# Kernel tuning notes

Hardware: AMD Instinct MI355X
Metric: run time of the kernel (lower is better)

The kernel has to match this reference:

```python
import jax, jax.numpy as jnp
import numpy as np

B, T, F = 1024, 256, 64
H1, H2, H3 = 64, 32, 16


def _lstm_params(key, in_dim, units, scale=0.1):
    k1, k2, k3 = jax.random.split(key, 3)
    W = jax.random.normal(k1, (in_dim, 4 * units), jnp.float32) * scale
    U = jax.random.normal(k2, (units, 4 * units), jnp.float32) * scale
    b = jax.random.normal(k3, (4 * units,), jnp.float32) * scale
    return W, U, b


def lstm_seq(x, W, U, b, reverse):
    """Keras-style LSTM (gate order i,f,g,o). Returns (all_h [B,T,H] time-aligned, last_h [B,H])."""
    Bx = x.shape[0]
    H = U.shape[0]
    xz = jnp.einsum('bti,ij->btj', x, W) + b  # [B,T,4H]
    if reverse:
        xz = xz[:, ::-1]
    xz = jnp.swapaxes(xz, 0, 1)  # [T,B,4H]

    def step(carry, zx):
        h, c = carry
        z = zx + h @ U
        i, f, g, o = jnp.split(z, 4, axis=-1)
        i = jax.nn.sigmoid(i)
        f = jax.nn.sigmoid(f)
        g = jnp.tanh(g)
        o = jax.nn.sigmoid(o)
        c = f * c + i * g
        h = o * jnp.tanh(c)
        return (h, c), h

    h0 = jnp.zeros((Bx, H), x.dtype)
    (hT, _), hs = jax.lax.scan(step, (h0, h0), xz)
    hs = jnp.swapaxes(hs, 0, 1)  # [B,T,H]
    if reverse:
        hs = hs[:, ::-1]  # Keras Bidirectional re-reverses backward outputs
    return hs, hT


def setup_inputs() -> dict:
    key = jax.random.key(0)
    ks = jax.random.split(key, 10)
    x = jax.random.normal(ks[0], (B, T, F), jnp.float32)
    W1f, U1f, b1f = _lstm_params(ks[1], F, H1)
    W1b, U1b, b1b = _lstm_params(ks[2], F, H1)
    W2f, U2f, b2f = _lstm_params(ks[3], 2 * H1, H2)
    W2b, U2b, b2b = _lstm_params(ks[4], 2 * H1, H2)
    W3f, U3f, b3f = _lstm_params(ks[5], 2 * H2, H3)
    W3b, U3b, b3b = _lstm_params(ks[6], 2 * H2, H3)
    Wd1 = jax.random.normal(ks[7], (2 * H3, 16), jnp.float32) * 0.1
    bd1 = jnp.zeros((16,), jnp.float32)
    Wd2 = jax.random.normal(ks[8], (16, 2), jnp.float32) * 0.1
    bd2 = jnp.zeros((2,), jnp.float32)
    return dict(inputs=x,
                W1f=W1f, U1f=U1f, b1f=b1f, W1b=W1b, U1b=U1b, b1b=b1b,
                W2f=W2f, U2f=U2f, b2f=b2f, W2b=W2b, U2b=U2b, b2b=b2b,
                W3f=W3f, U3f=U3f, b3f=b3f, W3b=W3b, U3b=U3b, b3b=b3b,
                Wd1=Wd1, bd1=bd1, Wd2=Wd2, bd2=bd2)


def reference(inputs,
              W1f, U1f, b1f, W1b, U1b, b1b,
              W2f, U2f, b2f, W2b, U2b, b2b,
              W3f, U3f, b3f, W3b, U3b, b3b,
              Wd1, bd1, Wd2, bd2):
    # inference path: all dropout / GaussianDropout layers are identity
    hf, _ = lstm_seq(inputs, W1f, U1f, b1f, reverse=False)
    hb, _ = lstm_seq(inputs, W1b, U1b, b1b, reverse=True)
    x = jnp.concatenate([hf, hb], axis=-1)  # [B,T,128]

    hf, _ = lstm_seq(x, W2f, U2f, b2f, reverse=False)
    hb, _ = lstm_seq(x, W2b, U2b, b2b, reverse=True)
    x = jnp.concatenate([hf, hb], axis=-1)  # [B,T,64]

    _, hf_last = lstm_seq(x, W3f, U3f, b3f, reverse=False)
    _, hb_last = lstm_seq(x, W3b, U3b, b3b, reverse=True)
    x = jnp.concatenate([hf_last, hb_last], axis=-1)  # [B,32] (Flatten is identity)

    x = jnp.clip(x @ Wd1 + bd1, 0.0, 6.0)  # relu6
    logits = x @ Wd2 + bd2
    return jax.nn.softmax(logits, axis=-1)
```

## Files before the change

### kernel.cpp

```cpp
#include <hip/hip_runtime.h>
#include <hip/hip_bf16.h>

#define T_SEQ 256
#define BATCH 1024

typedef __attribute__((ext_vector_type(8))) short  short8;
typedef __attribute__((ext_vector_type(4))) float  floatx4;
typedef unsigned short ushort_t;
typedef unsigned int   uint_t;

template <int P> struct IC { static constexpr int v = P; };

constexpr float NL2E = -1.4426950408889634f;
constexpr float L2E2 =  2.8853900817779268f;

__device__ __forceinline__ float exp2_fast(float x) {
    float r; asm("v_exp_f32 %0, %1" : "=v"(r) : "v"(x)); return r;
}
__device__ __forceinline__ float rcp_fast(float x) {
    float r; asm("v_rcp_f32 %0, %1" : "=v"(r) : "v"(x)); return r;
}
__device__ __forceinline__ ushort_t f2bf(float f) {
    union { float f; uint_t u; } v; v.f = f;
    uint_t r = v.u + 0x7FFFu + ((v.u >> 16) & 1u);
    return (ushort_t)(r >> 16);
}
__device__ __forceinline__ uint_t pk_bf16(float a, float b) {
    union { __hip_bfloat162 h; uint_t u; } v;
    v.h = __float22bfloat162_rn(make_float2(a, b));
    return v.u;
}
__device__ __forceinline__ void sync_lds() {
    asm volatile("s_waitcnt lgkmcnt(0)\n\ts_barrier" ::: "memory");
}


__device__ __forceinline__ void sig4(const float z[4], float o[4]) {
    const float A0 = 1.0f + exp2_fast(z[0]);
    const float A1 = 1.0f + exp2_fast(z[1]);
    const float A2 = 1.0f + exp2_fast(z[2]);
    const float A3 = 1.0f + exp2_fast(z[3]);
    const float P01 = A0 * A1, P23 = A2 * A3;
    const float R   = rcp_fast(P01 * P23);
    const float R01 = R * P23;
    const float R23 = R * P01;
    o[0] = R01 * A1; o[1] = R01 * A0;
    o[2] = R23 * A3; o[3] = R23 * A2;
}
__device__ __forceinline__ void tanh4(const float z[4], float o[4]) {
    float s[4]; sig4(z, s);
#pragma unroll
    for (int r = 0; r < 4; r++) o[r] = fmaf(-2.0f, s[r], 1.0f);
}

template <int D, int H, bool IS_FIRST, bool SEQ_OUT, int MODE>
__global__ __launch_bounds__(64 * (H / 16), 1) void lstm_fused(
    const void* __restrict__ xin,
    const float* __restrict__ Wf, const float* __restrict__ Uf, const float* __restrict__ bgf,
    const float* __restrict__ Wb, const float* __restrict__ Ub, const float* __restrict__ bgb,
    void* __restrict__ outp)
{
    constexpr bool SW = (MODE >= 1);
    constexpr int UG  = H / 16;
    constexpr int KSx = D / 32;
    constexpr int KSh = (H + 31) / 32;
    constexpr int HP  = (H < 32 ? 32 : H) + 8;
    constexpr int G4  = 4 * H;
    constexpr int NTH = 64 * UG;
    static_assert(D % 32 == 0 && T_SEQ % 4 == 0, "shape");

    const int tid  = threadIdx.x;
    const int ug   = tid >> 6;
    const int lane = tid & 63;
    const int lm   = lane & 15;
    const int lq   = lane >> 4;
    const int dir  = blockIdx.y;
    const int b0   = blockIdx.x * 16;

    const float* W  = dir ? Wb  : Wf;
    const float* U  = dir ? Ub  : Uf;
    const float* bg = dir ? bgb : bgf;

    __shared__ __align__(16) ushort_t hbuf[2 * 16 * HP];

    short8  aw[4][KSx];
    short8  hw[4][KSh];
    floatx4 bias4[4];
#pragma unroll
    for (int g = 0; g < 4; g++) {
        const float sc = (g == 2) ? L2E2 : NL2E;
        const int ub = g * H + ug * 16;
        floatx4 b4;
#pragma unroll
        for (int r = 0; r < 4; r++)
            b4[r] = sc * bg[ub + (SW ? lq * 4 + r : lm)];
        bias4[g] = b4;
        const int nc = ub + lm;
#pragma unroll
        for (int ks = 0; ks < KSx; ks++) {
            short8 f;
#pragma unroll
            for (int e = 0; e < 8; e++)
                f[e] = (short)f2bf(sc * W[(ks * 32 + lq * 8 + e) * G4 + nc]);
            aw[g][ks] = f;
        }
#pragma unroll
        for (int ks = 0; ks < KSh; ks++) {
            short8 f;
#pragma unroll
            for (int e = 0; e < 8; e++) {
                const int k = ks * 32 + lq * 8 + e;
                f[e] = (k < H) ? (short)f2bf(sc * U[k * G4 + nc]) : (short)0;
            }
            hw[g][ks] = f;
        }
    }

    for (int idx = tid; idx < 2 * 16 * HP; idx += NTH)
        hbuf[idx] = 0;

    float cst[4];
    float hl[4];
#pragma unroll
    for (int r = 0; r < 4; r++) { cst[r] = 0.f; hl[r] = 0.f; }

    const int t0 = dir ? T_SEQ - 1 : 0;
    const float*    pxf = (const float*)xin + ((size_t)(b0 + lm) * T_SEQ + t0) * D + lq * 8;
    const ushort_t* pxb = (const ushort_t*)xin + ((size_t)t0 * BATCH + b0 + lm) * D + lq * 8;
    const long xstepf = dir ? -(long)D : (long)D;
    const long xstepb = (dir ? -(long)BATCH : (long)BATCH) * D;
    ushort_t* pout;
    if constexpr (SW)
        pout = (ushort_t*)outp + ((size_t)t0 * BATCH + b0 + lm) * (2 * H) + dir * H +
               ug * 16 + lq * 4;
    else
        pout = (ushort_t*)outp + ((size_t)t0 * BATCH + b0 + lq * 4) * (2 * H) + dir * H +
               ug * 16 + lm;
    const long ostep = (dir ? -(long)BATCH : (long)BATCH) * (2 * H);

    float4 rawf[4][2 * KSx];
    short8 rawb[4][KSx];

    auto load_slot = [&](auto sl_) {
        constexpr int SL = decltype(sl_)::v;
        if (IS_FIRST) {
#pragma unroll
            for (int ks = 0; ks < KSx; ks++) {
                rawf[SL][2 * ks + 0] = *(const float4*)(pxf + ks * 32 + 0);
                rawf[SL][2 * ks + 1] = *(const float4*)(pxf + ks * 32 + 4);
            }
            pxf += xstepf;
        } else {
#pragma unroll
            for (int ks = 0; ks < KSx; ks++)
                rawb[SL][ks] = *(const short8*)(pxb + ks * 32);
            pxb += xstepb;
        }
    };

    load_slot(IC<0>{}); load_slot(IC<1>{}); load_slot(IC<2>{}); load_slot(IC<3>{});
    __syncthreads();

    auto step = [&](auto p_, auto sl_, int s) {
        constexpr int P  = decltype(p_)::v;
        constexpr int SL = decltype(sl_)::v;

        short8 fh[KSh];
#pragma unroll
        for (int ks = 0; ks < KSh; ks++)
            fh[ks] = *(const short8*)&hbuf[(P * 16 + lm) * HP + ks * 32 + lq * 8];

        short8 av[KSx];
        if (IS_FIRST) {
#pragma unroll
            for (int ks = 0; ks < KSx; ks++) {
                union { short8 s; uint_t u[4]; } f;
                const float* ra = (const float*)&rawf[SL][2 * ks];
#pragma unroll
                for (int e = 0; e < 4; e++) f.u[e] = pk_bf16(ra[2 * e], ra[2 * e + 1]);
                av[ks] = f.s;
            }
        } else {
#pragma unroll
            for (int ks = 0; ks < KSx; ks++) av[ks] = rawb[SL][ks];
        }

        floatx4 acc[4];
#pragma unroll
        for (int g = 0; g < 4; g++)
            acc[g] = SW
                ? __builtin_amdgcn_mfma_f32_16x16x32_bf16(aw[g][0], av[0], bias4[g], 0, 0, 0)
                : __builtin_amdgcn_mfma_f32_16x16x32_bf16(av[0], aw[g][0], bias4[g], 0, 0, 0);
#pragma unroll
        for (int ks = 1; ks < KSx; ks++)
#pragma unroll
            for (int g = 0; g < 4; g++)
                acc[g] = SW
                    ? __builtin_amdgcn_mfma_f32_16x16x32_bf16(aw[g][ks], av[ks], acc[g], 0, 0, 0)
                    : __builtin_amdgcn_mfma_f32_16x16x32_bf16(av[ks], aw[g][ks], acc[g], 0, 0, 0);

        if (s + 4 < T_SEQ) load_slot(sl_);

#pragma unroll
        for (int ks = 0; ks < KSh; ks++)
#pragma unroll
            for (int g = 0; g < 4; g++)
                acc[g] = SW
                    ? __builtin_amdgcn_mfma_f32_16x16x32_bf16(hw[g][ks], fh[ks], acc[g], 0, 0, 0)
                    : __builtin_amdgcn_mfma_f32_16x16x32_bf16(fh[ks], hw[g][ks], acc[g], 0, 0, 0);

        float zi[4], zf[4], zg[4], zo[4];
#pragma unroll
        for (int r = 0; r < 4; r++) {
            zi[r] = acc[0][r]; zf[r] = acc[1][r];
            zg[r] = acc[2][r]; zo[r] = acc[3][r];
        }
        float gi[4], gf[4], gg[4], go[4];
        sig4(zi, gi); sig4(zf, gf); tanh4(zg, gg); sig4(zo, go);
        float cz[4];
#pragma unroll
        for (int r = 0; r < 4; r++) {
            cst[r] = fmaf(gf[r], cst[r], L2E2 * (gi[r] * gg[r]));
            cz[r] = cst[r];
        }
        float tc[4];
        tanh4(cz, tc);
        float hv[4];
#pragma unroll
        for (int r = 0; r < 4; r++) hv[r] = go[r] * tc[r];

        if constexpr (SW) {
            const uint_t d0 = pk_bf16(hv[0], hv[1]);
            const uint_t d1 = pk_bf16(hv[2], hv[3]);
            uint2 wv; wv.x = d0; wv.y = d1;
            *(uint2*)&hbuf[((P ^ 1) * 16 + lm) * HP + ug * 16 + lq * 4] = wv;
            if (SEQ_OUT) {
                uint2 ov; ov.x = d0; ov.y = d1;
                *(uint2*)&pout[0] = ov;
            } else {
#pragma unroll
                for (int r = 0; r < 4; r++) hl[r] = hv[r];
            }
        } else {
#pragma unroll
            for (int r = 0; r < 4; r++) {
                const ushort_t hw_ = f2bf(hv[r]);
                hbuf[((P ^ 1) * 16 + lq * 4 + r) * HP + ug * 16 + lm] = hw_;
                if (SEQ_OUT) pout[r * 2 * H] = hw_;
                else         hl[r] = hv[r];
            }
        }
        pout += ostep;
        if (UG > 1) sync_lds();
    };

    for (int s = 0; s < T_SEQ; s += 4) {
        step(IC<0>{}, IC<0>{}, s);
        step(IC<1>{}, IC<1>{}, s + 1);
        step(IC<0>{}, IC<2>{}, s + 2);
        step(IC<1>{}, IC<3>{}, s + 3);
    }

    if (!SEQ_OUT) {
        float* op = (float*)outp;
        if constexpr (SW) {
            float4 v4 = make_float4(hl[0], hl[1], hl[2], hl[3]);
            *(float4*)&op[(size_t)(b0 + lm) * (2 * H) + dir * H + ug * 16 + lq * 4] = v4;
        } else {
#pragma unroll
            for (int r = 0; r < 4; r++)
                op[(size_t)(b0 + lq * 4 + r) * (2 * H) + dir * H + ug * 16 + lm] = hl[r];
        }
    }
}

__global__ __launch_bounds__(256) void dense_head(
    const float* __restrict__ h3, const float* __restrict__ Wd1, const float* __restrict__ bd1,
    const float* __restrict__ Wd2, const float* __restrict__ bd2, float* __restrict__ out)
{
    const int b = blockIdx.x * blockDim.x + threadIdx.x;
    if (b >= BATCH) return;
    float x[32];
#pragma unroll
    for (int k = 0; k < 32; k++) x[k] = h3[b * 32 + k];
    float y[16];
#pragma unroll
    for (int jj = 0; jj < 16; jj++) {
        float a = bd1[jj];
#pragma unroll
        for (int k = 0; k < 32; k++) a = fmaf(x[k], Wd1[k * 16 + jj], a);
        y[jj] = fminf(fmaxf(a, 0.0f), 6.0f);
    }
    float l0 = bd2[0], l1 = bd2[1];
#pragma unroll
    for (int k = 0; k < 16; k++) {
        l0 = fmaf(y[k], Wd2[k * 2 + 0], l0);
        l1 = fmaf(y[k], Wd2[k * 2 + 1], l1);
    }
    const float m = fmaxf(l0, l1);
    const float e0 = __expf(l0 - m), e1 = __expf(l1 - m);
    const float inv = 1.0f / (e0 + e1);
    out[b * 2 + 0] = e0 * inv;
    out[b * 2 + 1] = e1 * inv;
}

extern "C" void kernel_launch(void* const* d_in, const int* in_sizes, int n_in,
                              void* d_out, int out_size, void* d_ws, size_t ws_size,
                              hipStream_t stream)
{
    const float* x   = (const float*)d_in[0];
    const float* W1f = (const float*)d_in[1];
    const float* U1f = (const float*)d_in[2];
    const float* b1f = (const float*)d_in[3];
    const float* W1b = (const float*)d_in[4];
    const float* U1b = (const float*)d_in[5];
    const float* b1b = (const float*)d_in[6];
    const float* W2f = (const float*)d_in[7];
    const float* U2f = (const float*)d_in[8];
    const float* b2f = (const float*)d_in[9];
    const float* W2b = (const float*)d_in[10];
    const float* U2b = (const float*)d_in[11];
    const float* b2b = (const float*)d_in[12];
    const float* W3f = (const float*)d_in[13];
    const float* U3f = (const float*)d_in[14];
    const float* b3f = (const float*)d_in[15];
    const float* W3b = (const float*)d_in[16];
    const float* U3b = (const float*)d_in[17];
    const float* b3b = (const float*)d_in[18];
    const float* Wd1 = (const float*)d_in[19];
    const float* bd1 = (const float*)d_in[20];
    const float* Wd2 = (const float*)d_in[21];
    const float* bd2 = (const float*)d_in[22];

    char* ws = (char*)d_ws;
    void*  l1out = (void*)ws;
    void*  l2out = (void*)(ws + (size_t)64 * 1024 * 1024);
    float* h3    = (float*)(ws + (size_t)96 * 1024 * 1024);
    float* out   = (float*)d_out;

    dim3 grid(BATCH / 16, 2);

    lstm_fused<64, 64, true, true, 0>
        <<<grid, 256, 0, stream>>>(x, W1f, U1f, b1f, W1b, U1b, b1b, l1out);
    lstm_fused<128, 32, false, true, 1>
        <<<grid, 128, 0, stream>>>(l1out, W2f, U2f, b2f, W2b, U2b, b2b, l2out);
    lstm_fused<64, 16, false, false, 1>
        <<<grid, 64, 0, stream>>>(l2out, W3f, U3f, b3f, W3b, U3b, b3b, h3);
    dense_head<<<dim3(BATCH / 256), 256, 0, stream>>>(h3, Wd1, bd1, Wd2, bd2, out);
}
```

Baseline: 497.4 us.

## Add single-wave layer-3 LSTM kernel exchanging h via bpermute; per-element activations in layer 1

Adds a dedicated layer-3 kernel for the single-wave case. It passes the hidden state between lanes through ds_bpermute instead of an LDS buffer with barriers, and folds the bias into the MFMA accumulator init. It also adds an ACT template switch: layer 1 computes each sigmoid/tanh with its own reciprocal instead of the shared-reciprocal sig4 trick. This spends more transcendental instructions in exchange for shorter dependency chains. The new layer-3 path depends on the l2out layout being time-major bf16 and assumes the bpermute lane mapping matches the MFMA B-fragment layout.

```diff
diff --git a/kernel.cpp b/kernel.cpp
--- a/kernel.cpp
+++ b/kernel.cpp
@@ -53,7 +53,7 @@
     for (int r = 0; r < 4; r++) o[r] = fmaf(-2.0f, s[r], 1.0f);
 }
 
-template <int D, int H, bool IS_FIRST, bool SEQ_OUT, int MODE>
+template <int D, int H, bool IS_FIRST, bool SEQ_OUT, int MODE, int ACT>
 __global__ __launch_bounds__(64 * (H / 16), 1) void lstm_fused(
     const void* __restrict__ xin,
     const float* __restrict__ Wf, const float* __restrict__ Uf, const float* __restrict__ bgf,
@@ -209,25 +209,38 @@
                     ? __builtin_amdgcn_mfma_f32_16x16x32_bf16(hw[g][ks], fh[ks], acc[g], 0, 0, 0)
                     : __builtin_amdgcn_mfma_f32_16x16x32_bf16(fh[ks], hw[g][ks], acc[g], 0, 0, 0);
 
-        float zi[4], zf[4], zg[4], zo[4];
-#pragma unroll
-        for (int r = 0; r < 4; r++) {
-            zi[r] = acc[0][r]; zf[r] = acc[1][r];
-            zg[r] = acc[2][r]; zo[r] = acc[3][r];
-        }
-        float gi[4], gf[4], gg[4], go[4];
-        sig4(zi, gi); sig4(zf, gf); tanh4(zg, gg); sig4(zo, go);
-        float cz[4];
-#pragma unroll
-        for (int r = 0; r < 4; r++) {
-            cst[r] = fmaf(gf[r], cst[r], L2E2 * (gi[r] * gg[r]));
-            cz[r] = cst[r];
-        }
-        float tc[4];
-        tanh4(cz, tc);
         float hv[4];
-#pragma unroll
-        for (int r = 0; r < 4; r++) hv[r] = go[r] * tc[r];
+        if constexpr (ACT == 0) {
+#pragma unroll
+            for (int r = 0; r < 4; r++) {
+                const float gi = rcp_fast(1.0f + exp2_fast(acc[0][r]));
+                const float gf = rcp_fast(1.0f + exp2_fast(acc[1][r]));
+                const float gg = 1.0f - 2.0f * rcp_fast(1.0f + exp2_fast(acc[2][r]));
+                const float go = rcp_fast(1.0f + exp2_fast(acc[3][r]));
+                cst[r] = fmaf(gf, cst[r], L2E2 * (gi * gg));
+                const float tc = 1.0f - 2.0f * rcp_fast(1.0f + exp2_fast(cst[r]));
+                hv[r] = go * tc;
+            }
+        } else {
+            float zi[4], zf[4], zg[4], zo[4];
+#pragma unroll
+            for (int r = 0; r < 4; r++) {
+                zi[r] = acc[0][r]; zf[r] = acc[1][r];
+                zg[r] = acc[2][r]; zo[r] = acc[3][r];
+            }
+            float gi[4], gf[4], gg[4], go[4];
+            sig4(zi, gi); sig4(zf, gf); tanh4(zg, gg); sig4(zo, go);
+            float cz[4];
+#pragma unroll
+            for (int r = 0; r < 4; r++) {
+                cst[r] = fmaf(gf[r], cst[r], L2E2 * (gi[r] * gg[r]));
+                cz[r] = cst[r];
+            }
+            float tc[4];
+            tanh4(cz, tc);
+#pragma unroll
+            for (int r = 0; r < 4; r++) hv[r] = go[r] * tc[r];
+        }
 
         if constexpr (SW) {
             const uint_t d0 = pk_bf16(hv[0], hv[1]);
@@ -272,6 +285,136 @@
                 op[(size_t)(b0 + lq * 4 + r) * (2 * H) + dir * H + ug * 16 + lm] = hl[r];
         }
     }
+}
+
+template <int D, int H>
+__global__ __launch_bounds__(64, 1) void lstm_l3(
+    const ushort_t* __restrict__ xin,
+    const float* __restrict__ Wf, const float* __restrict__ Uf, const float* __restrict__ bgf,
+    const float* __restrict__ Wb, const float* __restrict__ Ub, const float* __restrict__ bgb,
+    float* __restrict__ outp)
+{
+    constexpr int KSx = D / 32;
+    constexpr int G4  = 4 * H;
+    static_assert(D % 32 == 0 && H == 16 && T_SEQ % 4 == 0, "l3 shape");
+
+    const int lane = threadIdx.x & 63;
+    const int lm   = lane & 15;
+    const int lq   = lane >> 4;
+    const int dir  = blockIdx.y;
+    const int b0   = blockIdx.x * 16;
+
+    const float* W  = dir ? Wb  : Wf;
+    const float* U  = dir ? Ub  : Uf;
+    const float* bg = dir ? bgb : bgf;
+
+    short8  aw[4][KSx];
+    short8  hw[4];
+    floatx4 bias4[4];
+#pragma unroll
+    for (int g = 0; g < 4; g++) {
+        const float sc = (g == 2) ? L2E2 : NL2E;
+        floatx4 b4;
+#pragma unroll
+        for (int r = 0; r < 4; r++) b4[r] = sc * bg[g * H + lq * 4 + r];
+        bias4[g] = b4;
+        const int nc = g * H + lm;
+#pragma unroll
+        for (int ks = 0; ks < KSx; ks++) {
+            short8 f;
+#pragma unroll
+            for (int e = 0; e < 8; e++)
+                f[e] = (short)f2bf(sc * W[(ks * 32 + lq * 8 + e) * G4 + nc]);
+            aw[g][ks] = f;
+        }
+        short8 f;
+#pragma unroll
+        for (int e = 0; e < 8; e++) {
+            const int k = lq * 8 + e;
+            f[e] = (k < H) ? (short)f2bf(sc * U[k * G4 + nc]) : (short)0;
+        }
+        hw[g] = f;
+    }
+
+    const int ia = (lm + 32 * (lq & 1)) * 4;
+    const int ib = ia + 64;
+
+    uint_t d0 = 0, d1 = 0;
+    float cst[4] = {0.f, 0.f, 0.f, 0.f};
+    float hl[4]  = {0.f, 0.f, 0.f, 0.f};
+
+    const int t0 = dir ? T_SEQ - 1 : 0;
+    const ushort_t* pxb = xin + ((size_t)t0 * BATCH + b0 + lm) * D + lq * 8;
+    const long xstepb = (dir ? -(long)BATCH : (long)BATCH) * D;
+
+    short8 rawb[4][KSx];
+    auto load_slot = [&](auto sl_) {
+        constexpr int SL = decltype(sl_)::v;
+#pragma unroll
+        for (int ks = 0; ks < KSx; ks++)
+            rawb[SL][ks] = *(const short8*)(pxb + ks * 32);
+        pxb += xstepb;
+    };
+    load_slot(IC<0>{}); load_slot(IC<1>{}); load_slot(IC<2>{}); load_slot(IC<3>{});
+
+    auto step = [&](auto sl_, int s) {
+        constexpr int SL = decltype(sl_)::v;
+
+        union { uint_t u[4]; short8 s8; } fr;
+        fr.u[0] = (uint_t)__builtin_amdgcn_ds_bpermute(ia, (int)d0);
+        fr.u[1] = (uint_t)__builtin_amdgcn_ds_bpermute(ia, (int)d1);
+        fr.u[2] = (uint_t)__builtin_amdgcn_ds_bpermute(ib, (int)d0);
+        fr.u[3] = (uint_t)__builtin_amdgcn_ds_bpermute(ib, (int)d1);
+
+        floatx4 acc[4];
+#pragma unroll
+        for (int g = 0; g < 4; g++)
+            acc[g] = __builtin_amdgcn_mfma_f32_16x16x32_bf16(aw[g][0], rawb[SL][0], bias4[g], 0, 0, 0);
+#pragma unroll
+        for (int ks = 1; ks < KSx; ks++)
+#pragma unroll
+            for (int g = 0; g < 4; g++)
+                acc[g] = __builtin_amdgcn_mfma_f32_16x16x32_bf16(aw[g][ks], rawb[SL][ks], acc[g], 0, 0, 0);
+
+        if (s + 4 < T_SEQ) load_slot(sl_);
+
+#pragma unroll
+        for (int g = 0; g < 4; g++)
+            acc[g] = __builtin_amdgcn_mfma_f32_16x16x32_bf16(hw[g], fr.s8, acc[g], 0, 0, 0);
+
+        float zi[4], zf[4], zg[4], zo[4];
+#pragma unroll
+        for (int r = 0; r < 4; r++) {
+            zi[r] = acc[0][r]; zf[r] = acc[1][r];
+            zg[r] = acc[2][r]; zo[r] = acc[3][r];
+        }
+        float gi[4], gf[4], gg[4], go[4];
+        sig4(zi, gi); sig4(zf, gf); tanh4(zg, gg); sig4(zo, go);
+        float cz[4];
+#pragma unroll
+        for (int r = 0; r < 4; r++) {
+            cst[r] = fmaf(gf[r], cst[r], L2E2 * (gi[r] * gg[r]));
+            cz[r] = cst[r];
+        }
+        float tc[4];
+        tanh4(cz, tc);
+        float hv[4];
+#pragma unroll
+        for (int r = 0; r < 4; r++) { hv[r] = go[r] * tc[r]; hl[r] = hv[r]; }
+
+        d0 = pk_bf16(hv[0], hv[1]);
+        d1 = pk_bf16(hv[2], hv[3]);
+    };
+
+    for (int s = 0; s < T_SEQ; s += 4) {
+        step(IC<0>{}, s);
+        step(IC<1>{}, s + 1);
+        step(IC<2>{}, s + 2);
+        step(IC<3>{}, s + 3);
+    }
+
+    float4 v4 = make_float4(hl[0], hl[1], hl[2], hl[3]);
+    *(float4*)&outp[(size_t)(b0 + lm) * (2 * H) + dir * H + lq * 4] = v4;
 }
 
 __global__ __launch_bounds__(256) void dense_head(
@@ -340,11 +483,11 @@
 
     dim3 grid(BATCH / 16, 2);
 
-    lstm_fused<64, 64, true, true, 0>
+    lstm_fused<64, 64, true, true, 0, 0>
         <<<grid, 256, 0, stream>>>(x, W1f, U1f, b1f, W1b, U1b, b1b, l1out);
-    lstm_fused<128, 32, false, true, 1>
+    lstm_fused<128, 32, false, true, 1, 1>
         <<<grid, 128, 0, stream>>>(l1out, W2f, U2f, b2f, W2b, U2b, b2b, l2out);
-    lstm_fused<64, 16, false, false, 1>
-        <<<grid, 64, 0, stream>>>(l2out, W3f, U3f, b3f, W3b, U3b, b3b, h3);
+    lstm_l3<64, 16>
+        <<<grid, 64, 0, stream>>>((const ushort_t*)l2out, W3f, U3f, b3f, W3b, U3b, b3b, h3);
     dense_head<<<dim3(BATCH / 256), 256, 0, stream>>>(h3, Wd1, bd1, Wd2, bd2, out);
 }
```

Measured after the change: 503.5 us. Within noise of the previous version (+1.2%).
